# Kernel optimization log

Measured on AMD Instinct MI355X. Metric: run time of the kernel, lower is better.

The kernel has to match this reference:

```python
import jax, jax.numpy as jnp
import numpy as np

T = 20000          # document length in tokens
EMBED_DIM = 300    # GloVe 840B.300d
STATE_DIM = 400    # 2 * lstm_dim (bidirectional)
HIDDEN = 150       # Scorer hidden_dim default
MAX_N = 10         # span widths 1..10
G_DIM = 2 * STATE_DIM + EMBED_DIM  # 1100


def _mlp3(x, W1, b1, W2, b2, W3, b3):
    # Scorer: Linear -> ReLU -> Linear -> ReLU -> Linear(->1)
    h = jax.nn.relu(x @ W1 + b1)
    h = jax.nn.relu(h @ W2 + b2)
    return h @ W3 + b3


def _span_features(embeds, states, attn_logits):
    """Vectorized SpanEncoder: for every window of width n in 1..MAX_N,
    softmax the per-token attention logits within the window, attention-pool
    the word embeddings, and concat [state_start, state_end, pooled].
    Returns g of shape [sum_n (T-n+1), G_DIM]."""
    gs = []
    for n in range(1, MAX_N + 1):
        S = T - n + 1  # number of width-n spans
        # [n, S] windowed logits and [n, S, E] windowed embeds via shifted slices
        a = jnp.stack([attn_logits[j:j + S] for j in range(n)], axis=0)
        w = jax.nn.softmax(a, axis=0)  # softmax within each span (dim=0 in torch)
        we = jnp.stack([embeds[j:j + S] for j in range(n)], axis=0)
        pooled = jnp.einsum('ns,nse->se', w, we)  # [S, E]
        g = jnp.concatenate([states[:S], states[n - 1:n - 1 + S], pooled], axis=-1)
        gs.append(g)
    return jnp.concatenate(gs, axis=0)


def setup_inputs() -> dict:
    key = jax.random.key(0)
    ks = jax.random.split(key, 16)
    sc = 0.05
    return {
        'embeds': jax.random.normal(ks[0], (T, EMBED_DIM), jnp.float32),
        'states': jax.random.normal(ks[1], (T, STATE_DIM), jnp.float32),
        'attn_W1': jax.random.normal(ks[2], (STATE_DIM, HIDDEN), jnp.float32) * sc,
        'attn_b1': jnp.zeros((HIDDEN,), jnp.float32),
        'attn_W2': jax.random.normal(ks[3], (HIDDEN, HIDDEN), jnp.float32) * sc,
        'attn_b2': jnp.zeros((HIDDEN,), jnp.float32),
        'attn_W3': jax.random.normal(ks[4], (HIDDEN, 1), jnp.float32) * sc,
        'attn_b3': jnp.zeros((1,), jnp.float32),
        'sc_W1': jax.random.normal(ks[5], (G_DIM, HIDDEN), jnp.float32) * sc,
        'sc_b1': jnp.zeros((HIDDEN,), jnp.float32),
        'sc_W2': jax.random.normal(ks[6], (HIDDEN, HIDDEN), jnp.float32) * sc,
        'sc_b2': jnp.zeros((HIDDEN,), jnp.float32),
        'sc_W3': jax.random.normal(ks[7], (HIDDEN, 1), jnp.float32) * sc,
        'sc_b3': jnp.zeros((1,), jnp.float32),
    }


def reference(embeds, states, attn_W1, attn_b1, attn_W2, attn_b2, attn_W3, attn_b3,
              sc_W1, sc_b1, sc_W2, sc_b2, sc_W3, sc_b3):
    # SpanAttention: per-token scalar attention logit from the BiLSTM state
    attn_logits = _mlp3(states, attn_W1, attn_b1, attn_W2, attn_b2, attn_W3, attn_b3)[:, 0]
    # SpanEncoder: ragged windowed attention pooling + boundary-state concat
    g = _span_features(embeds, states, attn_logits)  # [10T-45, 1100]
    # SpanScorer: MLP score per span
    scores = _mlp3(g, sc_W1, sc_b1, sc_W2, sc_b2, sc_W3, sc_b3)[:, 0]
    return scores
```

## Files before the change

kernel.cpp:

```cpp
#include <hip/hip_runtime.h>
#include <hip/hip_bf16.h>
#include <math.h>

#define T_LEN 20000
#define HID 150

typedef __attribute__((ext_vector_type(8))) __bf16 bf16x8;
typedef __attribute__((ext_vector_type(4))) float f32x4;

__device__ __forceinline__ short f2bf(float f) {
    unsigned u = __float_as_uint(f);
    u = (u + 0x7fff + ((u >> 16) & 1)) >> 16;
    return (short)u;
}

__device__ __forceinline__ unsigned pk2(float a, float b) {
    __hip_bfloat162 h = __float22bfloat162_rn(make_float2(a, b));
    return *(unsigned*)&h;
}

__device__ __forceinline__ bf16x8 cvt8(float4 a, float4 b) {
    union { unsigned u[4]; bf16x8 v; } r;
    r.u[0] = pk2(a.x, a.y);
    r.u[1] = pk2(a.z, a.w);
    r.u[2] = pk2(b.x, b.y);
    r.u[3] = pk2(b.z, b.w);
    return r.v;
}

__device__ __forceinline__ float2 ubf2(unsigned u) {
    return make_float2(__uint_as_float(u << 16),
                       __uint_as_float(u & 0xffff0000u));
}

__global__ __launch_bounds__(256) void wprep(
    const float* __restrict__ sc_W1, const float* __restrict__ attn_W1,
    const float* __restrict__ attn_W2, const float* __restrict__ sc_W2,
    short* __restrict__ frag)
{
    int t = blockIdx.x * 256 + threadIdx.x;
    if (t >= 302080) return;
    float v = 0.f;
    if (t < 199680) {
        int e = t & 7, g = t >> 3;
        int lane = g & 63, h = g >> 6;
        int ks = h % 13, nt = h / 13;
        int k = ks * 32 + (lane >> 4) * 8 + e;
        int cs = (nt % 10) * 16 + (lane & 15);
        if (k < 400 && cs < HID) {
            if (nt < 10)      v = sc_W1[(long)k * HID + cs];
            else if (nt < 20) v = sc_W1[(long)(400 + k) * HID + cs];
            else              v = attn_W1[(long)k * HID + cs];
        }
    } else if (t < 250880) {
        int r = t - 199680;
        int e = r & 7, g = r >> 3;
        int lane = g & 63, h = g >> 6;
        int ks = h % 10, nt = h / 10;
        int k = ks * 32 + (lane >> 4) * 8 + e;
        int cs = nt * 16 + (lane & 15);
        if (k < 300 && cs < HID) v = sc_W1[(long)(800 + k) * HID + cs];
    } else if (t < 276480) {
        int r = t - 250880;
        int e = r & 7, g = r >> 3;
        int lane = g & 63, h = g >> 6;
        int ks = h % 5, nt = h / 5;
        int k = ks * 32 + (lane >> 4) * 8 + e;
        int cs = nt * 16 + (lane & 15);
        if (k < HID && cs < HID) v = attn_W2[(long)k * HID + cs];
    } else {
        int r = t - 276480;
        int e = r & 7, g = r >> 3;
        int lane = g & 63, h = g >> 6;
        int ks = h % 5, nt = h / 5;
        int k = ks * 32 + (lane >> 4) * 8 + e;
        int cs = nt * 16 + (lane & 15);
        if (k < HID && cs < HID) v = sc_W2[(long)k * HID + cs];
    }
    frag[t] = f2bf(v);
}

__global__ __launch_bounds__(384, 3) void fusedAP(
    const float* __restrict__ states, const float* __restrict__ embeds,
    const short* __restrict__ frag,
    const float* __restrict__ scb1, const float* __restrict__ ab1,
    const float* __restrict__ ab2, const float* __restrict__ aW3,
    const float* __restrict__ ab3,
    short* __restrict__ Ubf, short* __restrict__ Vbf, short* __restrict__ Pbf,
    float* __restrict__ logits)
{
    __shared__ short As[2 * 13 * 64 * 8];
    __shared__ short h1s[32 * 168];
    __shared__ float red[32][6];
    __shared__ float sb1[160], ab1s[160];
    const int tid = threadIdx.x;
    const int w = tid >> 6, lane = tid & 63;
    const int ml = lane & 15, kg = lane >> 4;
    const int m0 = blockIdx.x * 32;

    for (int t = tid; t < 160; t += 384) {
        sb1[t]  = (t < HID) ? scb1[t] : 0.f;
        ab1s[t] = (t < HID) ? ab1[t]  : 0.f;
    }
    for (int idx = tid; idx < 2 * 13 * 64; idx += 384) {
        int g = idx / 832, r = idx - g * 832;
        int ks = r >> 6, l2 = r & 63;
        int k = ks * 32 + ((l2 >> 4) << 3);
        const float* Ar = states + (long)(m0 + g * 16 + (l2 & 15)) * 400;
        float4 a0 = make_float4(0.f, 0.f, 0.f, 0.f), a1 = a0;
        if (k + 4 <= 400) a0 = *(const float4*)&Ar[k];
        if (k + 8 <= 400) a1 = *(const float4*)&Ar[k + 4];
        *(bf16x8*)&As[idx * 8] = cvt8(a0, a1);
    }
    __syncthreads();

    f32x4 acc[5][2];
    #pragma unroll
    for (int t = 0; t < 5; ++t)
        #pragma unroll
        for (int g = 0; g < 2; ++g)
            acc[t][g] = (f32x4){0.f, 0.f, 0.f, 0.f};

    const short* fb = frag + lane * 8;
    const int t5 = w * 5;

    bf16x8 bcur[5], bnxt[5];
    #pragma unroll
    for (int t = 0; t < 5; ++t)
        bcur[t] = *(const bf16x8*)&fb[((t5 + t) * 13 + 0) << 9];

    #pragma unroll
    for (int ks = 0; ks < 13; ++ks) {
        if (ks < 12) {
            #pragma unroll
            for (int t = 0; t < 5; ++t)
                bnxt[t] = *(const bf16x8*)&fb[((t5 + t) * 13 + ks + 1) << 9];
        }
        bf16x8 af0 = *(const bf16x8*)&As[(ks * 64 + lane) * 8];
        bf16x8 af1 = *(const bf16x8*)&As[((832 + ks * 64) + lane) * 8];
        #pragma unroll
        for (int t = 0; t < 5; ++t) {
            acc[t][0] = __builtin_amdgcn_mfma_f32_16x16x32_bf16(bcur[t], af0, acc[t][0], 0, 0, 0);
            acc[t][1] = __builtin_amdgcn_mfma_f32_16x16x32_bf16(bcur[t], af1, acc[t][1], 0, 0, 0);
        }
        #pragma unroll
        for (int t = 0; t < 5; ++t) bcur[t] = bnxt[t];
    }

    #pragma unroll
    for (int t = 0; t < 5; ++t) {
        int nt = t5 + t;
        #pragma unroll
        for (int g = 0; g < 2; ++g) {
            if (w < 2) {
                int col0 = nt * 16 + kg * 4;
                float v[4];
                #pragma unroll
                for (int r = 0; r < 4; ++r) {
                    int c = col0 + r;
                    v[r] = (c < HID) ? acc[t][g][r] + sb1[c] : 0.f;
                }
                *(uint2*)&Ubf[(long)(m0 + g * 16 + ml) * 160 + col0] =
                    make_uint2(pk2(v[0], v[1]), pk2(v[2], v[3]));
            } else if (w < 4) {
                int col0 = (nt - 10) * 16 + kg * 4;
                float v[4];
                #pragma unroll
                for (int r = 0; r < 4; ++r) {
                    int c = col0 + r;
                    v[r] = (c < HID) ? acc[t][g][r] : 0.f;
                }
                *(uint2*)&Vbf[(long)(m0 + g * 16 + ml) * 160 + col0] =
                    make_uint2(pk2(v[0], v[1]), pk2(v[2], v[3]));
            } else {
                int col0 = (nt - 20) * 16 + kg * 4;
                float v[4];
                #pragma unroll
                for (int r = 0; r < 4; ++r) {
                    int c = col0 + r;
                    v[r] = (c < HID) ? fmaxf(acc[t][g][r] + ab1s[c], 0.f) : 0.f;
                }
                *(uint2*)&h1s[(g * 16 + ml) * 168 + col0] =
                    make_uint2(pk2(v[0], v[1]), pk2(v[2], v[3]));
            }
        }
    }
    __syncthreads();

    for (int idx = tid; idx < 2 * 10 * 64; idx += 384) {
        int g = idx / 640, r = idx - g * 640;
        int ks = r >> 6, l2 = r & 63;
        int k = ks * 32 + ((l2 >> 4) << 3);
        const float* Er = embeds + (long)(m0 + g * 16 + (l2 & 15)) * 300;
        float4 a0 = make_float4(0.f, 0.f, 0.f, 0.f), a1 = a0;
        if (k + 4 <= 300) a0 = *(const float4*)&Er[k];
        if (k + 8 <= 300) a1 = *(const float4*)&Er[k + 4];
        *(bf16x8*)&As[idx * 8] = cvt8(a0, a1);
    }
    __syncthreads();

    const int tB = (w < 4) ? 2 * w : (w == 4 ? 8 : 9);
    const int nTP = (w < 4) ? 2 : 1;
    {
        f32x4 accP[2][2];
        #pragma unroll
        for (int t = 0; t < 2; ++t)
            #pragma unroll
            for (int g = 0; g < 2; ++g)
                accP[t][g] = (f32x4){0.f, 0.f, 0.f, 0.f};

        const short* fP = frag + 199680 + lane * 8;
        bf16x8 pcur[2], pnxt[2];
        #pragma unroll
        for (int t = 0; t < 2; ++t)
            if (t < nTP) pcur[t] = *(const bf16x8*)&fP[((tB + t) * 10 + 0) << 9];

        #pragma unroll
        for (int ks = 0; ks < 10; ++ks) {
            if (ks < 9) {
                #pragma unroll
                for (int t = 0; t < 2; ++t)
                    if (t < nTP) pnxt[t] = *(const bf16x8*)&fP[((tB + t) * 10 + ks + 1) << 9];
            }
            bf16x8 af0 = *(const bf16x8*)&As[(ks * 64 + lane) * 8];
            bf16x8 af1 = *(const bf16x8*)&As[((640 + ks * 64) + lane) * 8];
            #pragma unroll
            for (int t = 0; t < 2; ++t) {
                if (t < nTP) {
                    accP[t][0] = __builtin_amdgcn_mfma_f32_16x16x32_bf16(pcur[t], af0, accP[t][0], 0, 0, 0);
                    accP[t][1] = __builtin_amdgcn_mfma_f32_16x16x32_bf16(pcur[t], af1, accP[t][1], 0, 0, 0);
                }
            }
            #pragma unroll
            for (int t = 0; t < 2; ++t) pcur[t] = pnxt[t];
        }

        #pragma unroll
        for (int t = 0; t < 2; ++t) {
            if (t < nTP) {
                int col0 = (tB + t) * 16 + kg * 4;
                #pragma unroll
                for (int g = 0; g < 2; ++g) {
                    float v[4];
                    #pragma unroll
                    for (int r = 0; r < 4; ++r) {
                        int c = col0 + r;
                        v[r] = (c < HID) ? accP[t][g][r] : 0.f;
                    }
                    *(uint2*)&Pbf[(long)(m0 + g * 16 + ml) * 160 + col0] =
                        make_uint2(pk2(v[0], v[1]), pk2(v[2], v[3]));
                }
            }
        }
    }

    const short* fAt2 = frag + 250880 + lane * 8;
    bf16x8 af2[2][5];
    #pragma unroll
    for (int g = 0; g < 2; ++g)
        #pragma unroll
        for (int ks = 0; ks < 5; ++ks)
            af2[g][ks] = *(const bf16x8*)&h1s[(g * 16 + ml) * 168 + ks * 32 + kg * 8];

    float score[2][4];
    #pragma unroll
    for (int g = 0; g < 2; ++g)
        #pragma unroll
        for (int r = 0; r < 4; ++r) score[g][r] = 0.f;

    #pragma unroll
    for (int t = 0; t < 2; ++t) {
        if (t < nTP) {
            int nt = tB + t;
            bf16x8 wb[5];
            #pragma unroll
            for (int ks = 0; ks < 5; ++ks)
                wb[ks] = *(const bf16x8*)&fAt2[(nt * 5 + ks) << 9];
            f32x4 a2[2];
            a2[0] = (f32x4){0.f, 0.f, 0.f, 0.f};
            a2[1] = (f32x4){0.f, 0.f, 0.f, 0.f};
            #pragma unroll
            for (int g = 0; g < 2; ++g)
                #pragma unroll
                for (int ks = 0; ks < 5; ++ks)
                    a2[g] = __builtin_amdgcn_mfma_f32_16x16x32_bf16(af2[g][ks], wb[ks], a2[g], 0, 0, 0);
            int col = nt * 16 + ml;
            float b2v = (col < HID) ? ab2[col] : 0.f;
            float w3v = (col < HID) ? aW3[col] : 0.f;
            #pragma unroll
            for (int g = 0; g < 2; ++g)
                #pragma unroll
                for (int r = 0; r < 4; ++r)
                    score[g][r] += fmaxf(a2[g][r] + b2v, 0.f) * w3v;
        }
    }
    #pragma unroll
    for (int g = 0; g < 2; ++g)
        #pragma unroll
        for (int r = 0; r < 4; ++r) {
            score[g][r] += __shfl_xor(score[g][r], 1);
            score[g][r] += __shfl_xor(score[g][r], 2);
            score[g][r] += __shfl_xor(score[g][r], 4);
            score[g][r] += __shfl_xor(score[g][r], 8);
        }
    if (ml == 0) {
        #pragma unroll
        for (int g = 0; g < 2; ++g)
            #pragma unroll
            for (int r = 0; r < 4; ++r)
                red[g * 16 + kg * 4 + r][w] = score[g][r];
    }
    __syncthreads();
    if (tid < 32)
        logits[m0 + tid] = red[tid][0] + red[tid][1] + red[tid][2] +
                           red[tid][3] + red[tid][4] + red[tid][5] + ab3[0];
}

__global__ __launch_bounds__(256) void span_all(
    const short* __restrict__ Ubf, const short* __restrict__ Vbf,
    const short* __restrict__ Pbf, const float* __restrict__ logits,
    const short* __restrict__ fW2, const float* __restrict__ b2,
    const float* __restrict__ W3, const float* __restrict__ b3,
    float* __restrict__ out)
{
    __shared__ short h1s[2][32 * 168];
    __shared__ float red[2][32][2];
    __shared__ float Ls[48], ebuf[48];
    __shared__ float b2s[160], W3s[160];

    const int tid = threadIdx.x;
    const int s0 = blockIdx.x * 32;
    const int nlo = blockIdx.y ? 6 : 1;
    const int nhi = blockIdx.y ? 10 : 5;

    if (tid < 48) {
        int r = s0 + tid; if (r > T_LEN - 1) r = T_LEN - 1;
        Ls[tid] = (tid < 41) ? logits[r] : -1e30f;
    }
    for (int t = tid; t < 160; t += 256) {
        b2s[t] = (t < HID) ? b2[t] : 0.f;
        W3s[t] = (t < HID) ? W3[t] : 0.f;
    }
    __syncthreads();
    if (tid < 48) {
        float M = -1e30f;
        for (int t = 0; t < 41; ++t) M = fmaxf(M, Ls[t]);
        ebuf[tid] = (tid < 41) ? expf(Ls[tid] - M) : 0.f;
    }
    __syncthreads();

    const int i = tid >> 3;
    const int q = tid & 7;
    const int d0 = 20 * q;
    const int s = s0 + i;
    int su = s; if (su > T_LEN - 1) su = T_LEN - 1;

    float Ur[20];
    {
        const uint2* U2 = (const uint2*)&Ubf[(long)su * 160 + d0];
        #pragma unroll
        for (int c = 0; c < 5; ++c) {
            uint2 uv = U2[c];
            float2 a = ubf2(uv.x), b_ = ubf2(uv.y);
            Ur[4 * c + 0] = a.x;  Ur[4 * c + 1] = a.y;
            Ur[4 * c + 2] = b_.x; Ur[4 * c + 3] = b_.y;
        }
    }
    float accp[20];
    #pragma unroll
    for (int d = 0; d < 20; ++d) accp[d] = 0.f;
    float den = 0.f;

    for (int j = 0; j < nlo - 1; ++j) {
        int rr_ = s + j; if (rr_ > T_LEN - 1) rr_ = T_LEN - 1;
        float e = ebuf[i + j];
        den += e;
        const uint2* P2 = (const uint2*)&Pbf[(long)rr_ * 160 + d0];
        #pragma unroll
        for (int c = 0; c < 5; ++c) {
            uint2 pv = P2[c];
            float2 a = ubf2(pv.x), b_ = ubf2(pv.y);
            accp[4 * c + 0] += e * a.x;  accp[4 * c + 1] += e * a.y;
            accp[4 * c + 2] += e * b_.x; accp[4 * c + 3] += e * b_.y;
        }
    }

    const int w = tid >> 6, lane = tid & 63;
    const int ml = lane & 15, kg = lane >> 4;
    const int mt = w >> 1;
    const int nt0 = (w & 1) * 5;
    const float bb = b3[0];

    auto phase1 = [&](int n, int p) {
        int rr_ = s + n - 1; if (rr_ > T_LEN - 1) rr_ = T_LEN - 1;
        float e = ebuf[i + n - 1];
        den += e;
        {
            const uint2* P2 = (const uint2*)&Pbf[(long)rr_ * 160 + d0];
            #pragma unroll
            for (int c = 0; c < 5; ++c) {
                uint2 pv = P2[c];
                float2 a = ubf2(pv.x), b_ = ubf2(pv.y);
                accp[4 * c + 0] += e * a.x;  accp[4 * c + 1] += e * a.y;
                accp[4 * c + 2] += e * b_.x; accp[4 * c + 3] += e * b_.y;
            }
        }
        float invd = 1.f / den;
        {
            const uint2* V2 = (const uint2*)&Vbf[(long)rr_ * 160 + d0];
            #pragma unroll
            for (int c = 0; c < 5; ++c) {
                uint2 vv = V2[c];
                float2 a = ubf2(vv.x), b_ = ubf2(vv.y);
                float x0 = fmaxf(Ur[4 * c + 0] + a.x  + accp[4 * c + 0] * invd, 0.f);
                float x1 = fmaxf(Ur[4 * c + 1] + a.y  + accp[4 * c + 1] * invd, 0.f);
                float x2 = fmaxf(Ur[4 * c + 2] + b_.x + accp[4 * c + 2] * invd, 0.f);
                float x3 = fmaxf(Ur[4 * c + 3] + b_.y + accp[4 * c + 3] * invd, 0.f);
                *(uint2*)&h1s[p][i * 168 + d0 + 4 * c] =
                    make_uint2(pk2(x0, x1), pk2(x2, x3));
            }
        }
    };

    phase1(nlo, 0);
    __syncthreads();

    for (int n = nlo; n <= nhi; ++n) {
        const int p = (n - nlo) & 1;
        if (n < nhi) phase1(n + 1, 1 - p);

        bf16x8 af[5];
        #pragma unroll
        for (int ks = 0; ks < 5; ++ks)
            af[ks] = *(const bf16x8*)&h1s[p][(mt * 16 + ml) * 168 + ks * 32 + kg * 8];

        float sc[4] = {0.f, 0.f, 0.f, 0.f};
        #pragma unroll
        for (int j = 0; j < 5; ++j) {
            int nt = nt0 + j;
            f32x4 a2 = {0.f, 0.f, 0.f, 0.f};
            #pragma unroll
            for (int ks = 0; ks < 5; ++ks) {
                bf16x8 bf = *(const bf16x8*)&fW2[(long)(((nt * 5 + ks) << 6) | lane) << 3];
                a2 = __builtin_amdgcn_mfma_f32_16x16x32_bf16(af[ks], bf, a2, 0, 0, 0);
            }
            int col = nt * 16 + ml;
            float b2v = b2s[col], w3v = W3s[col];
            #pragma unroll
            for (int r = 0; r < 4; ++r)
                sc[r] += fmaxf(a2[r] + b2v, 0.f) * w3v;
        }
        #pragma unroll
        for (int r = 0; r < 4; ++r) {
            sc[r] += __shfl_xor(sc[r], 1);
            sc[r] += __shfl_xor(sc[r], 2);
            sc[r] += __shfl_xor(sc[r], 4);
            sc[r] += __shfl_xor(sc[r], 8);
        }
        if (ml == 0) {
            #pragma unroll
            for (int r = 0; r < 4; ++r)
                red[p][mt * 16 + kg * 4 + r][w & 1] = sc[r];
        }
        __syncthreads();
        if (tid < 32) {
            int S = T_LEN - n + 1;
            int off = (n - 1) * (T_LEN + 1) - (n - 1) * n / 2;
            int sr = s0 + tid;
            if (sr < S) out[off + sr] = red[p][tid][0] + red[p][tid][1] + bb;
        }
    }
}

extern "C" void kernel_launch(void* const* d_in, const int* in_sizes, int n_in,
                              void* d_out, int out_size, void* d_ws, size_t ws_size,
                              hipStream_t stream) {
    const float* embeds  = (const float*)d_in[0];
    const float* states  = (const float*)d_in[1];
    const float* attn_W1 = (const float*)d_in[2];
    const float* attn_b1 = (const float*)d_in[3];
    const float* attn_W2 = (const float*)d_in[4];
    const float* attn_b2 = (const float*)d_in[5];
    const float* attn_W3 = (const float*)d_in[6];
    const float* attn_b3 = (const float*)d_in[7];
    const float* sc_W1   = (const float*)d_in[8];
    const float* sc_b1   = (const float*)d_in[9];
    const float* sc_W2   = (const float*)d_in[10];
    const float* sc_b2   = (const float*)d_in[11];
    const float* sc_W3   = (const float*)d_in[12];
    const float* sc_b3   = (const float*)d_in[13];
    float* out = (float*)d_out;

    short* wsS = (short*)d_ws;
    short* Ubf = wsS;
    short* Vbf = wsS + 3200256;
    short* Pbf = wsS + 6400512;
    short* frag = wsS + 9600768;
    float* logits = (float*)(wsS + 9902848);

    wprep<<<1180, 256, 0, stream>>>(sc_W1, attn_W1, attn_W2, sc_W2, frag);
    fusedAP<<<625, 384, 0, stream>>>(states, embeds, frag, sc_b1, attn_b1,
                                     attn_b2, attn_W3, attn_b3,
                                     Ubf, Vbf, Pbf, logits);
    span_all<<<dim3(625, 2), 256, 0, stream>>>(Ubf, Vbf, Pbf, logits,
                                               frag + 276480, sc_b2, sc_W3, sc_b3,
                                               out);
}
```

Before: 199.9 us.

## Fuse per-token projection and span scorer into one kernel with halo recompute

Merges the token-projection kernel and the span-scoring kernel into one kernel. Each block now recomputes U/V/P projections and attention logits for 48 rows (32 plus a 16-row halo), so the U, V, P intermediates and logits stay in shared memory instead of passing through global memory. Inside the span loop the block is warp-specialized: two warps build the next width's hidden layer while four warps run the second MLP layer with MFMA, double-buffered across the ten widths. The trade-off is about 50% redundant projection work for the halo, more shared memory per block, and a single block covering all ten widths where the old grid split them across two blocks, which may lower occupancy.

```diff
diff --git a/kernel.cpp b/kernel.cpp
--- a/kernel.cpp
+++ b/kernel.cpp
@@ -4,6 +4,7 @@
 
 #define T_LEN 20000
 #define HID 150
+#define STR 168
 
 typedef __attribute__((ext_vector_type(8))) __bf16 bf16x8;
 typedef __attribute__((ext_vector_type(4))) float f32x4;
@@ -80,140 +81,157 @@
     frag[t] = f2bf(v);
 }
 
-__global__ __launch_bounds__(384, 3) void fusedAP(
+__global__ __launch_bounds__(384) void mega(
     const float* __restrict__ states, const float* __restrict__ embeds,
     const short* __restrict__ frag,
     const float* __restrict__ scb1, const float* __restrict__ ab1,
     const float* __restrict__ ab2, const float* __restrict__ aW3,
     const float* __restrict__ ab3,
-    short* __restrict__ Ubf, short* __restrict__ Vbf, short* __restrict__ Pbf,
-    float* __restrict__ logits)
+    const float* __restrict__ b2, const float* __restrict__ W3,
+    const float* __restrict__ b3,
+    float* __restrict__ out)
 {
-    __shared__ short As[2 * 13 * 64 * 8];
-    __shared__ short h1s[32 * 168];
-    __shared__ float red[32][6];
-    __shared__ float sb1[160], ab1s[160];
+    __shared__ short AsU[19968];
+    __shared__ short Us[32 * STR];
+    __shared__ short Vs[48 * STR];
+    __shared__ short Ps[48 * STR];
+    __shared__ short X1s[48 * STR];
+    __shared__ float redl[48][6];
+    __shared__ float reds[2][32][2];
+    __shared__ float Ls[48], ebuf[48];
+    __shared__ float sb1[160], ab1s[160], b2s[160], W3s[160];
+
     const int tid = threadIdx.x;
     const int w = tid >> 6, lane = tid & 63;
     const int ml = lane & 15, kg = lane >> 4;
-    const int m0 = blockIdx.x * 32;
+    const int s0 = blockIdx.x * 32;
 
     for (int t = tid; t < 160; t += 384) {
         sb1[t]  = (t < HID) ? scb1[t] : 0.f;
         ab1s[t] = (t < HID) ? ab1[t]  : 0.f;
-    }
-    for (int idx = tid; idx < 2 * 13 * 64; idx += 384) {
+        b2s[t]  = (t < HID) ? b2[t]   : 0.f;
+        W3s[t]  = (t < HID) ? W3[t]   : 0.f;
+    }
+
+    for (int idx = tid; idx < 2496; idx += 384) {
         int g = idx / 832, r = idx - g * 832;
         int ks = r >> 6, l2 = r & 63;
         int k = ks * 32 + ((l2 >> 4) << 3);
-        const float* Ar = states + (long)(m0 + g * 16 + (l2 & 15)) * 400;
+        int row = s0 + g * 16 + (l2 & 15); if (row > T_LEN - 1) row = T_LEN - 1;
+        const float* Ar = states + (long)row * 400;
         float4 a0 = make_float4(0.f, 0.f, 0.f, 0.f), a1 = a0;
         if (k + 4 <= 400) a0 = *(const float4*)&Ar[k];
         if (k + 8 <= 400) a1 = *(const float4*)&Ar[k + 4];
-        *(bf16x8*)&As[idx * 8] = cvt8(a0, a1);
-    }
-    __syncthreads();
-
-    f32x4 acc[5][2];
-    #pragma unroll
-    for (int t = 0; t < 5; ++t)
-        #pragma unroll
-        for (int g = 0; g < 2; ++g)
-            acc[t][g] = (f32x4){0.f, 0.f, 0.f, 0.f};
-
-    const short* fb = frag + lane * 8;
-    const int t5 = w * 5;
-
-    bf16x8 bcur[5], bnxt[5];
-    #pragma unroll
-    for (int t = 0; t < 5; ++t)
-        bcur[t] = *(const bf16x8*)&fb[((t5 + t) * 13 + 0) << 9];
-
-    #pragma unroll
-    for (int ks = 0; ks < 13; ++ks) {
-        if (ks < 12) {
-            #pragma unroll
-            for (int t = 0; t < 5; ++t)
-                bnxt[t] = *(const bf16x8*)&fb[((t5 + t) * 13 + ks + 1) << 9];
-        }
-        bf16x8 af0 = *(const bf16x8*)&As[(ks * 64 + lane) * 8];
-        bf16x8 af1 = *(const bf16x8*)&As[((832 + ks * 64) + lane) * 8];
+        *(bf16x8*)&AsU[idx * 8] = cvt8(a0, a1);
+    }
+    __syncthreads();
+
+    {
+        f32x4 acc[5][3];
+        #pragma unroll
+        for (int t = 0; t < 5; ++t)
+            #pragma unroll
+            for (int g = 0; g < 3; ++g)
+                acc[t][g] = (f32x4){0.f, 0.f, 0.f, 0.f};
+
+        const short* fb = frag + lane * 8;
+        const int t5 = w * 5;
+        bf16x8 bcur[5], bnxt[5];
+        #pragma unroll
+        for (int t = 0; t < 5; ++t)
+            bcur[t] = *(const bf16x8*)&fb[((t5 + t) * 13) << 9];
+
+        #pragma unroll
+        for (int ks = 0; ks < 13; ++ks) {
+            if (ks < 12) {
+                #pragma unroll
+                for (int t = 0; t < 5; ++t)
+                    bnxt[t] = *(const bf16x8*)&fb[((t5 + t) * 13 + ks + 1) << 9];
+            }
+            bf16x8 af0 = *(const bf16x8*)&AsU[(ks * 64 + lane) * 8];
+            bf16x8 af1 = *(const bf16x8*)&AsU[(832 + ks * 64 + lane) * 8];
+            bf16x8 af2_ = *(const bf16x8*)&AsU[(1664 + ks * 64 + lane) * 8];
+            #pragma unroll
+            for (int t = 0; t < 5; ++t) {
+                acc[t][0] = __builtin_amdgcn_mfma_f32_16x16x32_bf16(bcur[t], af0, acc[t][0], 0, 0, 0);
+                acc[t][1] = __builtin_amdgcn_mfma_f32_16x16x32_bf16(bcur[t], af1, acc[t][1], 0, 0, 0);
+                acc[t][2] = __builtin_amdgcn_mfma_f32_16x16x32_bf16(bcur[t], af2_, acc[t][2], 0, 0, 0);
+            }
+            #pragma unroll
+            for (int t = 0; t < 5; ++t) bcur[t] = bnxt[t];
+        }
+
         #pragma unroll
         for (int t = 0; t < 5; ++t) {
-            acc[t][0] = __builtin_amdgcn_mfma_f32_16x16x32_bf16(bcur[t], af0, acc[t][0], 0, 0, 0);
-            acc[t][1] = __builtin_amdgcn_mfma_f32_16x16x32_bf16(bcur[t], af1, acc[t][1], 0, 0, 0);
-        }
-        #pragma unroll
-        for (int t = 0; t < 5; ++t) bcur[t] = bnxt[t];
-    }
-
-    #pragma unroll
-    for (int t = 0; t < 5; ++t) {
-        int nt = t5 + t;
-        #pragma unroll
-        for (int g = 0; g < 2; ++g) {
-            if (w < 2) {
-                int col0 = nt * 16 + kg * 4;
-                float v[4];
-                #pragma unroll
-                for (int r = 0; r < 4; ++r) {
-                    int c = col0 + r;
-                    v[r] = (c < HID) ? acc[t][g][r] + sb1[c] : 0.f;
+            int nt = t5 + t;
+            #pragma unroll
+            for (int g = 0; g < 3; ++g) {
+                if (w < 2) {
+                    if (g < 2) {
+                        int col0 = nt * 16 + kg * 4;
+                        float v[4];
+                        #pragma unroll
+                        for (int r = 0; r < 4; ++r) {
+                            int c = col0 + r;
+                            v[r] = (c < HID) ? acc[t][g][r] + sb1[c] : 0.f;
+                        }
+                        *(uint2*)&Us[(g * 16 + ml) * STR + col0] =
+                            make_uint2(pk2(v[0], v[1]), pk2(v[2], v[3]));
+                    }
+                } else if (w < 4) {
+                    int col0 = (nt - 10) * 16 + kg * 4;
+                    float v[4];
+                    #pragma unroll
+                    for (int r = 0; r < 4; ++r) {
+                        int c = col0 + r;
+                        v[r] = (c < HID) ? acc[t][g][r] : 0.f;
+                    }
+                    *(uint2*)&Vs[(g * 16 + ml) * STR + col0] =
+                        make_uint2(pk2(v[0], v[1]), pk2(v[2], v[3]));
+                } else {
+                    int col0 = (nt - 20) * 16 + kg * 4;
+                    float v[4];
+                    #pragma unroll
+                    for (int r = 0; r < 4; ++r) {
+                        int c = col0 + r;
+                        v[r] = (c < HID) ? fmaxf(acc[t][g][r] + ab1s[c], 0.f) : 0.f;
+                    }
+                    *(uint2*)&X1s[(g * 16 + ml) * STR + col0] =
+                        make_uint2(pk2(v[0], v[1]), pk2(v[2], v[3]));
                 }
-                *(uint2*)&Ubf[(long)(m0 + g * 16 + ml) * 160 + col0] =
-                    make_uint2(pk2(v[0], v[1]), pk2(v[2], v[3]));
-            } else if (w < 4) {
-                int col0 = (nt - 10) * 16 + kg * 4;
-                float v[4];
-                #pragma unroll
-                for (int r = 0; r < 4; ++r) {
-                    int c = col0 + r;
-                    v[r] = (c < HID) ? acc[t][g][r] : 0.f;
-                }
-                *(uint2*)&Vbf[(long)(m0 + g * 16 + ml) * 160 + col0] =
-                    make_uint2(pk2(v[0], v[1]), pk2(v[2], v[3]));
-            } else {
-                int col0 = (nt - 20) * 16 + kg * 4;
-                float v[4];
-                #pragma unroll
-                for (int r = 0; r < 4; ++r) {
-                    int c = col0 + r;
-                    v[r] = (c < HID) ? fmaxf(acc[t][g][r] + ab1s[c], 0.f) : 0.f;
-                }
-                *(uint2*)&h1s[(g * 16 + ml) * 168 + col0] =
-                    make_uint2(pk2(v[0], v[1]), pk2(v[2], v[3]));
-            }
-        }
-    }
-    __syncthreads();
-
-    for (int idx = tid; idx < 2 * 10 * 64; idx += 384) {
+            }
+        }
+    }
+    __syncthreads();
+
+    for (int idx = tid; idx < 1920; idx += 384) {
         int g = idx / 640, r = idx - g * 640;
         int ks = r >> 6, l2 = r & 63;
         int k = ks * 32 + ((l2 >> 4) << 3);
-        const float* Er = embeds + (long)(m0 + g * 16 + (l2 & 15)) * 300;
+        int row = s0 + g * 16 + (l2 & 15); if (row > T_LEN - 1) row = T_LEN - 1;
+        const float* Er = embeds + (long)row * 300;
         float4 a0 = make_float4(0.f, 0.f, 0.f, 0.f), a1 = a0;
         if (k + 4 <= 300) a0 = *(const float4*)&Er[k];
         if (k + 8 <= 300) a1 = *(const float4*)&Er[k + 4];
-        *(bf16x8*)&As[idx * 8] = cvt8(a0, a1);
+        *(bf16x8*)&AsU[idx * 8] = cvt8(a0, a1);
     }
     __syncthreads();
 
     const int tB = (w < 4) ? 2 * w : (w == 4 ? 8 : 9);
     const int nTP = (w < 4) ? 2 : 1;
     {
-        f32x4 accP[2][2];
+        f32x4 accP[2][3];
         #pragma unroll
         for (int t = 0; t < 2; ++t)
             #pragma unroll
-            for (int g = 0; g < 2; ++g)
+            for (int g = 0; g < 3; ++g)
                 accP[t][g] = (f32x4){0.f, 0.f, 0.f, 0.f};
 
         const short* fP = frag + 199680 + lane * 8;
         bf16x8 pcur[2], pnxt[2];
         #pragma unroll
         for (int t = 0; t < 2; ++t)
-            if (t < nTP) pcur[t] = *(const bf16x8*)&fP[((tB + t) * 10 + 0) << 9];
+            if (t < nTP) pcur[t] = *(const bf16x8*)&fP[((tB + t) * 10) << 9];
 
         #pragma unroll
         for (int ks = 0; ks < 10; ++ks) {
@@ -222,13 +240,15 @@
                 for (int t = 0; t < 2; ++t)
                     if (t < nTP) pnxt[t] = *(const bf16x8*)&fP[((tB + t) * 10 + ks + 1) << 9];
             }
-            bf16x8 af0 = *(const bf16x8*)&As[(ks * 64 + lane) * 8];
-            bf16x8 af1 = *(const bf16x8*)&As[((640 + ks * 64) + lane) * 8];
+            bf16x8 af0 = *(const bf16x8*)&AsU[(ks * 64 + lane) * 8];
+            bf16x8 af1 = *(const bf16x8*)&AsU[(640 + ks * 64 + lane) * 8];
+            bf16x8 af2_ = *(const bf16x8*)&AsU[(1280 + ks * 64 + lane) * 8];
             #pragma unroll
             for (int t = 0; t < 2; ++t) {
                 if (t < nTP) {
                     accP[t][0] = __builtin_amdgcn_mfma_f32_16x16x32_bf16(pcur[t], af0, accP[t][0], 0, 0, 0);
                     accP[t][1] = __builtin_amdgcn_mfma_f32_16x16x32_bf16(pcur[t], af1, accP[t][1], 0, 0, 0);
+                    accP[t][2] = __builtin_amdgcn_mfma_f32_16x16x32_bf16(pcur[t], af2_, accP[t][2], 0, 0, 0);
                 }
             }
             #pragma unroll
@@ -240,234 +260,201 @@
             if (t < nTP) {
                 int col0 = (tB + t) * 16 + kg * 4;
                 #pragma unroll
-                for (int g = 0; g < 2; ++g) {
+                for (int g = 0; g < 3; ++g) {
                     float v[4];
                     #pragma unroll
                     for (int r = 0; r < 4; ++r) {
                         int c = col0 + r;
                         v[r] = (c < HID) ? accP[t][g][r] : 0.f;
                     }
-                    *(uint2*)&Pbf[(long)(m0 + g * 16 + ml) * 160 + col0] =
+                    *(uint2*)&Ps[(g * 16 + ml) * STR + col0] =
                         make_uint2(pk2(v[0], v[1]), pk2(v[2], v[3]));
                 }
             }
         }
     }
 
-    const short* fAt2 = frag + 250880 + lane * 8;
-    bf16x8 af2[2][5];
-    #pragma unroll
-    for (int g = 0; g < 2; ++g)
-        #pragma unroll
-        for (int ks = 0; ks < 5; ++ks)
-            af2[g][ks] = *(const bf16x8*)&h1s[(g * 16 + ml) * 168 + ks * 32 + kg * 8];
-
-    float score[2][4];
-    #pragma unroll
-    for (int g = 0; g < 2; ++g)
-        #pragma unroll
-        for (int r = 0; r < 4; ++r) score[g][r] = 0.f;
-
-    #pragma unroll
-    for (int t = 0; t < 2; ++t) {
-        if (t < nTP) {
-            int nt = tB + t;
-            bf16x8 wb[5];
+    {
+        const short* fAt2 = frag + 250880 + lane * 8;
+        bf16x8 afx[3][5];
+        #pragma unroll
+        for (int g = 0; g < 3; ++g)
             #pragma unroll
             for (int ks = 0; ks < 5; ++ks)
-                wb[ks] = *(const bf16x8*)&fAt2[(nt * 5 + ks) << 9];
-            f32x4 a2[2];
-            a2[0] = (f32x4){0.f, 0.f, 0.f, 0.f};
-            a2[1] = (f32x4){0.f, 0.f, 0.f, 0.f};
-            #pragma unroll
-            for (int g = 0; g < 2; ++g)
+                afx[g][ks] = *(const bf16x8*)&X1s[(g * 16 + ml) * STR + ks * 32 + kg * 8];
+
+        float score[3][4];
+        #pragma unroll
+        for (int g = 0; g < 3; ++g)
+            #pragma unroll
+            for (int r = 0; r < 4; ++r) score[g][r] = 0.f;
+
+        #pragma unroll
+        for (int t = 0; t < 2; ++t) {
+            if (t < nTP) {
+                int nt = tB + t;
+                bf16x8 wb[5];
                 #pragma unroll
                 for (int ks = 0; ks < 5; ++ks)
-                    a2[g] = __builtin_amdgcn_mfma_f32_16x16x32_bf16(af2[g][ks], wb[ks], a2[g], 0, 0, 0);
-            int col = nt * 16 + ml;
-            float b2v = (col < HID) ? ab2[col] : 0.f;
-            float w3v = (col < HID) ? aW3[col] : 0.f;
-            #pragma unroll
-            for (int g = 0; g < 2; ++g)
+                    wb[ks] = *(const bf16x8*)&fAt2[(nt * 5 + ks) << 9];
+                f32x4 a2[3];
+                a2[0] = (f32x4){0.f, 0.f, 0.f, 0.f};
+                a2[1] = (f32x4){0.f, 0.f, 0.f, 0.f};
+                a2[2] = (f32x4){0.f, 0.f, 0.f, 0.f};
+                #pragma unroll
+                for (int g = 0; g < 3; ++g)
+                    #pragma unroll
+                    for (int ks = 0; ks < 5; ++ks)
+                        a2[g] = __builtin_amdgcn_mfma_f32_16x16x32_bf16(afx[g][ks], wb[ks], a2[g], 0, 0, 0);
+                int col = nt * 16 + ml;
+                float b2v = (col < HID) ? ab2[col] : 0.f;
+                float w3v = (col < HID) ? aW3[col] : 0.f;
+                #pragma unroll
+                for (int g = 0; g < 3; ++g)
+                    #pragma unroll
+                    for (int r = 0; r < 4; ++r)
+                        score[g][r] += fmaxf(a2[g][r] + b2v, 0.f) * w3v;
+            }
+        }
+        #pragma unroll
+        for (int g = 0; g < 3; ++g)
+            #pragma unroll
+            for (int r = 0; r < 4; ++r) {
+                score[g][r] += __shfl_xor(score[g][r], 1);
+                score[g][r] += __shfl_xor(score[g][r], 2);
+                score[g][r] += __shfl_xor(score[g][r], 4);
+                score[g][r] += __shfl_xor(score[g][r], 8);
+            }
+        if (ml == 0) {
+            #pragma unroll
+            for (int g = 0; g < 3; ++g)
                 #pragma unroll
                 for (int r = 0; r < 4; ++r)
-                    score[g][r] += fmaxf(a2[g][r] + b2v, 0.f) * w3v;
-        }
-    }
-    #pragma unroll
-    for (int g = 0; g < 2; ++g)
-        #pragma unroll
-        for (int r = 0; r < 4; ++r) {
-            score[g][r] += __shfl_xor(score[g][r], 1);
-            score[g][r] += __shfl_xor(score[g][r], 2);
-            score[g][r] += __shfl_xor(score[g][r], 4);
-            score[g][r] += __shfl_xor(score[g][r], 8);
-        }
-    if (ml == 0) {
-        #pragma unroll
-        for (int g = 0; g < 2; ++g)
-            #pragma unroll
-            for (int r = 0; r < 4; ++r)
-                red[g * 16 + kg * 4 + r][w] = score[g][r];
-    }
-    __syncthreads();
-    if (tid < 32)
-        logits[m0 + tid] = red[tid][0] + red[tid][1] + red[tid][2] +
-                           red[tid][3] + red[tid][4] + red[tid][5] + ab3[0];
-}
-
-__global__ __launch_bounds__(256) void span_all(
-    const short* __restrict__ Ubf, const short* __restrict__ Vbf,
-    const short* __restrict__ Pbf, const float* __restrict__ logits,
-    const short* __restrict__ fW2, const float* __restrict__ b2,
-    const float* __restrict__ W3, const float* __restrict__ b3,
-    float* __restrict__ out)
-{
-    __shared__ short h1s[2][32 * 168];
-    __shared__ float red[2][32][2];
-    __shared__ float Ls[48], ebuf[48];
-    __shared__ float b2s[160], W3s[160];
-
-    const int tid = threadIdx.x;
-    const int s0 = blockIdx.x * 32;
-    const int nlo = blockIdx.y ? 6 : 1;
-    const int nhi = blockIdx.y ? 10 : 5;
+                    redl[g * 16 + kg * 4 + r][w] = score[g][r];
+        }
+    }
+    __syncthreads();
 
     if (tid < 48) {
-        int r = s0 + tid; if (r > T_LEN - 1) r = T_LEN - 1;
-        Ls[tid] = (tid < 41) ? logits[r] : -1e30f;
-    }
-    for (int t = tid; t < 160; t += 256) {
-        b2s[t] = (t < HID) ? b2[t] : 0.f;
-        W3s[t] = (t < HID) ? W3[t] : 0.f;
-    }
-    __syncthreads();
+        float Lv = redl[tid][0] + redl[tid][1] + redl[tid][2] +
+                   redl[tid][3] + redl[tid][4] + redl[tid][5] + ab3[0];
+        Ls[tid] = (tid < 41) ? Lv : -1e30f;
+    }
     if (tid < 48) {
         float M = -1e30f;
         for (int t = 0; t < 41; ++t) M = fmaxf(M, Ls[t]);
         ebuf[tid] = (tid < 41) ? expf(Ls[tid] - M) : 0.f;
     }
-    __syncthreads();
-
-    const int i = tid >> 3;
-    const int q = tid & 7;
-    const int d0 = 20 * q;
-    const int s = s0 + i;
-    int su = s; if (su > T_LEN - 1) su = T_LEN - 1;
-
-    float Ur[20];
-    {
-        const uint2* U2 = (const uint2*)&Ubf[(long)su * 160 + d0];
-        #pragma unroll
-        for (int c = 0; c < 5; ++c) {
-            uint2 uv = U2[c];
-            float2 a = ubf2(uv.x), b_ = ubf2(uv.y);
-            Ur[4 * c + 0] = a.x;  Ur[4 * c + 1] = a.y;
-            Ur[4 * c + 2] = b_.x; Ur[4 * c + 3] = b_.y;
-        }
-    }
-    float accp[20];
-    #pragma unroll
-    for (int d = 0; d < 20; ++d) accp[d] = 0.f;
-    float den = 0.f;
-
-    for (int j = 0; j < nlo - 1; ++j) {
-        int rr_ = s + j; if (rr_ > T_LEN - 1) rr_ = T_LEN - 1;
-        float e = ebuf[i + j];
-        den += e;
-        const uint2* P2 = (const uint2*)&Pbf[(long)rr_ * 160 + d0];
-        #pragma unroll
-        for (int c = 0; c < 5; ++c) {
-            uint2 pv = P2[c];
-            float2 a = ubf2(pv.x), b_ = ubf2(pv.y);
-            accp[4 * c + 0] += e * a.x;  accp[4 * c + 1] += e * a.y;
-            accp[4 * c + 2] += e * b_.x; accp[4 * c + 3] += e * b_.y;
-        }
-    }
-
-    const int w = tid >> 6, lane = tid & 63;
-    const int ml = lane & 15, kg = lane >> 4;
-    const int mt = w >> 1;
-    const int nt0 = (w & 1) * 5;
-    const float bb = b3[0];
+
+    float Ur[2][20], accp[2][20], den[2];
+    const int u = tid & 127;
+    if (w >= 4) {
+        #pragma unroll
+        for (int z = 0; z < 2; ++z) {
+            int uz = u + z * 128;
+            int iz = uz >> 3, d0z = 20 * (uz & 7);
+            const uint2* U2 = (const uint2*)&Us[iz * STR + d0z];
+            #pragma unroll
+            for (int c = 0; c < 5; ++c) {
+                uint2 uv = U2[c];
+                float2 a = ubf2(uv.x), b_ = ubf2(uv.y);
+                Ur[z][4 * c + 0] = a.x;  Ur[z][4 * c + 1] = a.y;
+                Ur[z][4 * c + 2] = b_.x; Ur[z][4 * c + 3] = b_.y;
+            }
+            #pragma unroll
+            for (int d = 0; d < 20; ++d) accp[z][d] = 0.f;
+            den[z] = 0.f;
+        }
+    }
+    __syncthreads();
+
+    short* h1p = AsU;
 
     auto phase1 = [&](int n, int p) {
-        int rr_ = s + n - 1; if (rr_ > T_LEN - 1) rr_ = T_LEN - 1;
-        float e = ebuf[i + n - 1];
-        den += e;
-        {
-            const uint2* P2 = (const uint2*)&Pbf[(long)rr_ * 160 + d0];
+        #pragma unroll
+        for (int z = 0; z < 2; ++z) {
+            int uz = u + z * 128;
+            int iz = uz >> 3, d0z = 20 * (uz & 7);
+            int l = iz + n - 1;
+            float e = ebuf[l];
+            den[z] += e;
+            const uint2* P2 = (const uint2*)&Ps[l * STR + d0z];
             #pragma unroll
             for (int c = 0; c < 5; ++c) {
                 uint2 pv = P2[c];
                 float2 a = ubf2(pv.x), b_ = ubf2(pv.y);
-                accp[4 * c + 0] += e * a.x;  accp[4 * c + 1] += e * a.y;
-                accp[4 * c + 2] += e * b_.x; accp[4 * c + 3] += e * b_.y;
-            }
-        }
-        float invd = 1.f / den;
-        {
-            const uint2* V2 = (const uint2*)&Vbf[(long)rr_ * 160 + d0];
+                accp[z][4 * c + 0] += e * a.x;  accp[z][4 * c + 1] += e * a.y;
+                accp[z][4 * c + 2] += e * b_.x; accp[z][4 * c + 3] += e * b_.y;
+            }
+            float invd = 1.f / den[z];
+            const uint2* V2 = (const uint2*)&Vs[l * STR + d0z];
             #pragma unroll
             for (int c = 0; c < 5; ++c) {
                 uint2 vv = V2[c];
                 float2 a = ubf2(vv.x), b_ = ubf2(vv.y);
-                float x0 = fmaxf(Ur[4 * c + 0] + a.x  + accp[4 * c + 0] * invd, 0.f);
-                float x1 = fmaxf(Ur[4 * c + 1] + a.y  + accp[4 * c + 1] * invd, 0.f);
-                float x2 = fmaxf(Ur[4 * c + 2] + b_.x + accp[4 * c + 2] * invd, 0.f);
-                float x3 = fmaxf(Ur[4 * c + 3] + b_.y + accp[4 * c + 3] * invd, 0.f);
-                *(uint2*)&h1s[p][i * 168 + d0 + 4 * c] =
+                float x0 = fmaxf(Ur[z][4 * c + 0] + a.x  + accp[z][4 * c + 0] * invd, 0.f);
+                float x1 = fmaxf(Ur[z][4 * c + 1] + a.y  + accp[z][4 * c + 1] * invd, 0.f);
+                float x2 = fmaxf(Ur[z][4 * c + 2] + b_.x + accp[z][4 * c + 2] * invd, 0.f);
+                float x3 = fmaxf(Ur[z][4 * c + 3] + b_.y + accp[z][4 * c + 3] * invd, 0.f);
+                *(uint2*)&h1p[p * (32 * STR) + iz * STR + d0z + 4 * c] =
                     make_uint2(pk2(x0, x1), pk2(x2, x3));
             }
         }
     };
 
-    phase1(nlo, 0);
-    __syncthreads();
-
-    for (int n = nlo; n <= nhi; ++n) {
-        const int p = (n - nlo) & 1;
-        if (n < nhi) phase1(n + 1, 1 - p);
-
-        bf16x8 af[5];
-        #pragma unroll
-        for (int ks = 0; ks < 5; ++ks)
-            af[ks] = *(const bf16x8*)&h1s[p][(mt * 16 + ml) * 168 + ks * 32 + kg * 8];
-
-        float sc[4] = {0.f, 0.f, 0.f, 0.f};
-        #pragma unroll
-        for (int j = 0; j < 5; ++j) {
-            int nt = nt0 + j;
-            f32x4 a2 = {0.f, 0.f, 0.f, 0.f};
-            #pragma unroll
-            for (int ks = 0; ks < 5; ++ks) {
-                bf16x8 bf = *(const bf16x8*)&fW2[(long)(((nt * 5 + ks) << 6) | lane) << 3];
-                a2 = __builtin_amdgcn_mfma_f32_16x16x32_bf16(af[ks], bf, a2, 0, 0, 0);
-            }
-            int col = nt * 16 + ml;
-            float b2v = b2s[col], w3v = W3s[col];
-            #pragma unroll
-            for (int r = 0; r < 4; ++r)
-                sc[r] += fmaxf(a2[r] + b2v, 0.f) * w3v;
-        }
-        #pragma unroll
-        for (int r = 0; r < 4; ++r) {
-            sc[r] += __shfl_xor(sc[r], 1);
-            sc[r] += __shfl_xor(sc[r], 2);
-            sc[r] += __shfl_xor(sc[r], 4);
-            sc[r] += __shfl_xor(sc[r], 8);
-        }
-        if (ml == 0) {
-            #pragma unroll
-            for (int r = 0; r < 4; ++r)
-                red[p][mt * 16 + kg * 4 + r][w & 1] = sc[r];
+    if (w >= 4) phase1(1, 0);
+    __syncthreads();
+
+    const int mt = w >> 1;
+    const int nt0 = (w & 1) * 5;
+    const short* fW2 = frag + 276480;
+    const float bb = b3[0];
+
+    for (int n = 1; n <= 10; ++n) {
+        const int p = (n - 1) & 1;
+        if (w >= 4) {
+            if (n < 10) phase1(n + 1, 1 - p);
+        } else {
+            bf16x8 af[5];
+            #pragma unroll
+            for (int ks = 0; ks < 5; ++ks)
+                af[ks] = *(const bf16x8*)&h1p[p * (32 * STR) + (mt * 16 + ml) * STR + ks * 32 + kg * 8];
+
+            float sc[4] = {0.f, 0.f, 0.f, 0.f};
+            #pragma unroll
+            for (int j = 0; j < 5; ++j) {
+                int nt = nt0 + j;
+                f32x4 a2 = {0.f, 0.f, 0.f, 0.f};
+                #pragma unroll
+                for (int ks = 0; ks < 5; ++ks) {
+                    bf16x8 bf = *(const bf16x8*)&fW2[(long)(((nt * 5 + ks) << 6) | lane) << 3];
+                    a2 = __builtin_amdgcn_mfma_f32_16x16x32_bf16(af[ks], bf, a2, 0, 0, 0);
+                }
+                int col = nt * 16 + ml;
+                float b2v = b2s[col], w3v = W3s[col];
+                #pragma unroll
+                for (int r = 0; r < 4; ++r)
+                    sc[r] += fmaxf(a2[r] + b2v, 0.f) * w3v;
+            }
+            #pragma unroll
+            for (int r = 0; r < 4; ++r) {
+                sc[r] += __shfl_xor(sc[r], 1);
+                sc[r] += __shfl_xor(sc[r], 2);
+                sc[r] += __shfl_xor(sc[r], 4);
+                sc[r] += __shfl_xor(sc[r], 8);
+            }
+            if (ml == 0) {
+                #pragma unroll
+                for (int r = 0; r < 4; ++r)
+                    reds[p][mt * 16 + kg * 4 + r][w & 1] = sc[r];
+            }
         }
         __syncthreads();
         if (tid < 32) {
             int S = T_LEN - n + 1;
             int off = (n - 1) * (T_LEN + 1) - (n - 1) * n / 2;
             int sr = s0 + tid;
-            if (sr < S) out[off + sr] = red[p][tid][0] + red[p][tid][1] + bb;
+            if (sr < S) out[off + sr] = reds[p][tid][0] + reds[p][tid][1] + bb;
         }
     }
 }
@@ -491,18 +478,10 @@
     const float* sc_b3   = (const float*)d_in[13];
     float* out = (float*)d_out;
 
-    short* wsS = (short*)d_ws;
-    short* Ubf = wsS;
-    short* Vbf = wsS + 3200256;
-    short* Pbf = wsS + 6400512;
-    short* frag = wsS + 9600768;
-    float* logits = (float*)(wsS + 9902848);
+    short* frag = (short*)d_ws;
 
     wprep<<<1180, 256, 0, stream>>>(sc_W1, attn_W1, attn_W2, sc_W2, frag);
-    fusedAP<<<625, 384, 0, stream>>>(states, embeds, frag, sc_b1, attn_b1,
-                                     attn_b2, attn_W3, attn_b3,
-                                     Ubf, Vbf, Pbf, logits);
-    span_all<<<dim3(625, 2), 256, 0, stream>>>(Ubf, Vbf, Pbf, logits,
-                                               frag + 276480, sc_b2, sc_W3, sc_b3,
-                                               out);
-}
+    mega<<<625, 384, 0, stream>>>(states, embeds, frag, sc_b1, attn_b1,
+                                  attn_b2, attn_W3, attn_b3,
+                                  sc_b2, sc_W3, sc_b3, out);
+}
```

Measured after the change: 230.2 us. 15.2% more time.
